# Kernel optimization log

Measured on AMD Instinct MI355X. Metric: run time of the kernel, lower is better.

Reference implementation:

```python
import jax, jax.numpy as jnp
import numpy as np

B, S, NT, D, NU = 1024, 200, 10000, 256, 100000
BETA_1 = 0.1


def setup_inputs() -> dict:
    key = jax.random.key(0)
    ks = jax.random.split(key, 6)
    user_id = jax.random.randint(ks[0], (B,), 0, NU)
    event_type = jax.random.randint(ks[1], (B, S), 0, NT + 1)  # 0 = pad
    adjacent_matrix = jax.random.uniform(ks[2], (NT, NT), dtype=jnp.float32)
    pop_encoding = jax.random.normal(ks[3], (NT + 1, D), dtype=jnp.float32)
    event_emb = jax.random.normal(ks[4], (NT + 1, D), dtype=jnp.float32) * 0.02
    user_emb = jax.random.normal(ks[5], (NU, D), dtype=jnp.float32) * 0.02
    return dict(user_id=user_id, event_type=event_type,
                adjacent_matrix=adjacent_matrix, pop_encoding=pop_encoding,
                evaluation=0, event_emb=event_emb, user_emb=user_emb)


def _l2norm(x, eps):
    # tf.nn.l2_normalize: x * rsqrt(max(sum(x^2), eps))
    return x * jax.lax.rsqrt(jnp.maximum(jnp.sum(x * x, axis=-1, keepdims=True), eps))


def reference(user_id, event_type, adjacent_matrix, pop_encoding, evaluation, event_emb, user_emb):
    non_pad = (event_type != 0).astype(jnp.float32)[..., None]          # [B,S,1]
    enc = event_emb[event_type]                                          # [B,S,D]
    usr = user_emb[user_id]                                              # [B,D]
    pop = pop_encoding[event_type] * non_pad                             # [B,S,D]
    # enc += sign(enc) * l2_normalize(user_output) (default eps 1e-12)
    enc = enc + jnp.sign(enc) * _l2norm(usr, 1e-12)[:, None, :]
    # per-sample adjacency: two-axis gather of the item-item matrix
    idx = jnp.where(event_type > 0, event_type - 1, 0)                   # [B,S]
    adj = adjacent_matrix[idx[:, :, None], idx[:, None, :]]              # [B,S,S]
    has_valid = (jnp.sum(event_type > 0, axis=1) > 0).astype(jnp.float32)
    adj = adj * has_valid[:, None, None]  # rows with all-pad stay zero, as in the loop
    output = jnp.mean(enc, axis=1)                                       # [B,D]
    user_embeddings = jnp.concatenate([output, jnp.mean(pop, axis=1) * BETA_1], axis=-1)  # [B,2D]
    if evaluation:
        item_encoding = event_emb[1:]                                    # [NT,D]
        scores = user_embeddings[:, :D] @ item_encoding.T
    else:
        item_encoding = jnp.concatenate([event_emb[1:], pop_encoding[1:] * BETA_1], axis=-1)  # [NT,2D]
        scores = user_embeddings @ item_encoding.T                       # [B,NT]
    prediction = jnp.tanh(_l2norm(scores, 1e-05))
    return prediction, user_embeddings, pop, adj
```

## Files before the change

### kernel.cpp

```cpp
#include <hip/hip_runtime.h>
#include <math.h>

#define NB 1024
#define NS 200
#define NTOK 10000
#define ND 256
#define BETA 0.1f

static constexpr size_t PRED_OFF = 0;
static constexpr size_t UE_OFF   = (size_t)NB * NTOK;
static constexpr size_t POP_OFF  = UE_OFF + (size_t)NB * 2 * ND;
static constexpr size_t ADJ_OFF  = POP_OFF + (size_t)NB * NS * ND;

static constexpr size_t WS_SIDX   = 0;
static constexpr size_t WS_HV     = WS_SIDX + (size_t)NB * NS;
static constexpr size_t WS_COUNTS = WS_HV + NB;
static constexpr size_t WS_OFFS   = WS_COUNTS + NTOK;
static constexpr size_t WS_CURSOR = WS_OFFS + NTOK + 1;
static constexpr size_t WS_PAIRS  = WS_CURSOR + NTOK;
static constexpr size_t WS_UEBF   = 440640;
static constexpr size_t WS_IEBF   = WS_UEBF + 262144;

typedef __attribute__((ext_vector_type(8))) short bf16x8;
typedef __attribute__((ext_vector_type(4))) float f32x4;

static __device__ inline unsigned short f2bf(float f) {
    unsigned int u = __float_as_uint(f);
    return (unsigned short)((u + 0x7fffu + ((u >> 16) & 1u)) >> 16);
}

__global__ __launch_bounds__(256) void k_embed(
    const int* __restrict__ user_id,
    const int* __restrict__ event_type,
    const float* __restrict__ pop_encoding,
    const float* __restrict__ event_emb,
    const float* __restrict__ user_emb,
    float* __restrict__ ue,
    unsigned short* __restrict__ ue_bf,
    float* __restrict__ pop)
{
    const int b  = blockIdx.x;
    const int t  = threadIdx.x;
    const int sg = t >> 6;
    const int tl = t & 63;

    const int uid = user_id[b];
    const float4 u4 = *(const float4*)&user_emb[(size_t)uid * ND + tl * 4];

    float ss = u4.x * u4.x + u4.y * u4.y + u4.z * u4.z + u4.w * u4.w;
    #pragma unroll
    for (int o = 32; o > 0; o >>= 1) ss += __shfl_xor(ss, o, 64);
    const float rn = rsqrtf(fmaxf(ss, 1e-12f));
    const float4 nu4 = {u4.x * rn, u4.y * rn, u4.z * rn, u4.w * rn};

    __shared__ int et_s[NS];
    if (t < NS) et_s[t] = event_type[(size_t)b * NS + t];
    __syncthreads();

    float4 eacc = {0.f, 0.f, 0.f, 0.f};
    float4 pacc = {0.f, 0.f, 0.f, 0.f};
    #pragma unroll 2
    for (int it = 0; it < NS / 4; ++it) {
        const int s  = sg + 4 * it;
        const int et = et_s[s];
        const float4 e = *(const float4*)&event_emb[(size_t)et * ND + tl * 4];
        float4 p = *(const float4*)&pop_encoding[(size_t)et * ND + tl * 4];
        const float z = (et != 0) ? 1.f : 0.f;
        p.x *= z; p.y *= z; p.z *= z; p.w *= z;
        eacc.x += e.x + ((e.x > 0.f) ? nu4.x : ((e.x < 0.f) ? -nu4.x : 0.f));
        eacc.y += e.y + ((e.y > 0.f) ? nu4.y : ((e.y < 0.f) ? -nu4.y : 0.f));
        eacc.z += e.z + ((e.z > 0.f) ? nu4.z : ((e.z < 0.f) ? -nu4.z : 0.f));
        eacc.w += e.w + ((e.w > 0.f) ? nu4.w : ((e.w < 0.f) ? -nu4.w : 0.f));
        pacc.x += p.x; pacc.y += p.y; pacc.z += p.z; pacc.w += p.w;
        const f32x4 pv = {p.x, p.y, p.z, p.w};
        __builtin_nontemporal_store(pv, (f32x4*)&pop[((size_t)b * NS + s) * ND + tl * 4]);
    }

    __shared__ __align__(16) float4 es[4][64];
    __shared__ __align__(16) float4 ps[4][64];
    es[sg][tl] = eacc;
    ps[sg][tl] = pacc;
    __syncthreads();

    if (t < 64) {
        float4 ef = es[0][t], pf = ps[0][t];
        #pragma unroll
        for (int w = 1; w < 4; ++w) {
            const float4 e2 = es[w][t], p2 = ps[w][t];
            ef.x += e2.x; ef.y += e2.y; ef.z += e2.z; ef.w += e2.w;
            pf.x += p2.x; pf.y += p2.y; pf.z += p2.z; pf.w += p2.w;
        }
        const float se = 1.f / NS, sp = BETA / NS;
        const float4 eo = {ef.x * se, ef.y * se, ef.z * se, ef.w * se};
        const float4 po = {pf.x * sp, pf.y * sp, pf.z * sp, pf.w * sp};
        *(float4*)&ue[(size_t)b * 512 + t * 4]       = eo;
        *(float4*)&ue[(size_t)b * 512 + 256 + t * 4] = po;
        ushort4 he = {f2bf(eo.x), f2bf(eo.y), f2bf(eo.z), f2bf(eo.w)};
        ushort4 hp = {f2bf(po.x), f2bf(po.y), f2bf(po.z), f2bf(po.w)};
        *(ushort4*)&ue_bf[(size_t)b * 512 + t * 4]       = he;
        *(ushort4*)&ue_bf[(size_t)b * 512 + 256 + t * 4] = hp;
    }
}

__global__ __launch_bounds__(256) void k_iebf(
    const float* __restrict__ ee,
    const float* __restrict__ pe,
    unsigned short* __restrict__ ie)
{
    const int idx = blockIdx.x * 256 + threadIdx.x;
    if (idx >= NTOK * 128) return;
    const int row = idx >> 7;
    const int kq  = idx & 127;
    float4 v; float sc;
    if (kq < 64) { v = *(const float4*)&ee[(size_t)(row + 1) * ND + kq * 4]; sc = 1.f; }
    else         { v = *(const float4*)&pe[(size_t)(row + 1) * ND + (kq - 64) * 4]; sc = BETA; }
    ushort4 h = {f2bf(v.x * sc), f2bf(v.y * sc), f2bf(v.z * sc), f2bf(v.w * sc)};
    *(ushort4*)&ie[(size_t)row * 512 + kq * 4] = h;
}

__global__ __launch_bounds__(256) void k_zero(int* __restrict__ counts)
{
    const int i = blockIdx.x * 256 + threadIdx.x;
    if (i < NTOK) counts[i] = 0;
}

__global__ __launch_bounds__(256) void k_prep(
    const int* __restrict__ event_type,
    int* __restrict__ sidx_all,
    float* __restrict__ hvf,
    int* __restrict__ counts)
{
    const int b = blockIdx.x;
    const int t = threadIdx.x;
    __shared__ int hv_s;
    if (t == 0) hv_s = 0;
    __syncthreads();
    if (t < NS) {
        const int et = event_type[(size_t)b * NS + t];
        const int r  = (et > 0) ? (et - 1) : 0;
        sidx_all[(size_t)b * NS + t] = r;
        if (et > 0) hv_s = 1;
        atomicAdd(&counts[r], 1);
    }
    __syncthreads();
    if (t == 0) hvf[b] = hv_s ? 1.f : 0.f;
}

#define SCAN_CHUNK 40
__global__ __launch_bounds__(256) void k_scan(
    const int* __restrict__ counts,
    int* __restrict__ offsets,
    int* __restrict__ cursor)
{
    const int t = threadIdx.x;
    int sum = 0;
    int local[SCAN_CHUNK];
    #pragma unroll
    for (int k = 0; k < SCAN_CHUNK; ++k) {
        const int idx = t * SCAN_CHUNK + k;
        const int c = (idx < NTOK) ? counts[idx] : 0;
        local[k] = c;
        sum += c;
    }
    __shared__ int part[256];
    part[t] = sum;
    __syncthreads();
    for (int o = 1; o < 256; o <<= 1) {
        const int v = (t >= o) ? part[t - o] : 0;
        __syncthreads();
        part[t] += v;
        __syncthreads();
    }
    int running = part[t] - sum;
    #pragma unroll
    for (int k = 0; k < SCAN_CHUNK; ++k) {
        const int idx = t * SCAN_CHUNK + k;
        if (idx < NTOK) {
            offsets[idx] = running;
            cursor[idx]  = running;
            running += local[k];
        }
    }
    if (t == 255) offsets[NTOK] = part[255];
}

__global__ __launch_bounds__(256) void k_scatter(
    const int* __restrict__ sidx_all,
    int* __restrict__ cursor,
    int* __restrict__ pairs)
{
    const int b = blockIdx.x;
    const int t = threadIdx.x;
    if (t < NS) {
        const int r = sidx_all[(size_t)b * NS + t];
        const int slot = atomicAdd(&cursor[r], 1);
        pairs[slot] = b * NS + t;
    }
}

__global__ __launch_bounds__(256) void k_adj2(
    const float* __restrict__ A,
    const int* __restrict__ sidx_all,
    const int* __restrict__ offsets,
    const int* __restrict__ pairs,
    const float* __restrict__ hvf,
    float* __restrict__ adj)
{
    const int r = blockIdx.x;
    const int t = threadIdx.x;
    const int p0 = offsets[r];
    const int n  = offsets[r + 1] - p0;
    if (n == 0) return;

    __shared__ __align__(16) float rowlds[NTOK];
    const float4* Arow = (const float4*)(A + (size_t)r * NTOK);
    #pragma unroll 4
    for (int l = t; l < NTOK / 4; l += 256)
        ((float4*)rowlds)[l] = Arow[l];
    __syncthreads();

    const int wave = t >> 6, lane = t & 63;
    for (int pi = wave; pi < n; pi += 4) {
        const int pv = pairs[p0 + pi];
        const int b  = pv / NS;
        const float hv = hvf[b];
        if (lane < 50) {
            const int4 c4 = *(const int4*)&sidx_all[(size_t)b * NS + lane * 4];
            f32x4 v;
            v.x = rowlds[c4.x] * hv;
            v.y = rowlds[c4.y] * hv;
            v.z = rowlds[c4.z] * hv;
            v.w = rowlds[c4.w] * hv;
            __builtin_nontemporal_store(v, (f32x4*)&adj[(size_t)pv * NS + lane * 4]);
        }
    }
}

#define GBM 128
#define GBN 128
#define GBK 32
#define LDK 40

__global__ __launch_bounds__(256) void k_gemm_mfma(
    const unsigned short* __restrict__ ue_bf,
    const unsigned short* __restrict__ ie_bf,
    float* __restrict__ scores)
{
    __shared__ __align__(16) unsigned short As[GBM * LDK];
    __shared__ __align__(16) unsigned short Bs[GBN * LDK];

    const int t  = threadIdx.x;
    const int bn = blockIdx.x, bm = blockIdx.y;
    const int m0 = bm * GBM, n0 = bn * GBN;

    const int wave = t >> 6, lane = t & 63;
    const int ww = wave & 1, wm = wave >> 1;
    const int lr = lane & 15;
    const int kg = lane >> 4;

    const int kq = t & 7;
    const int rq = t >> 3;

    f32x4 acc[4][4] = {};

    for (int k0 = 0; k0 < 512; k0 += GBK) {
        #pragma unroll
        for (int i = 0; i < 4; ++i) {
            const int r = rq + 32 * i;
            *(ushort4*)&As[r * LDK + kq * 4] =
                *(const ushort4*)&ue_bf[(size_t)(m0 + r) * 512 + k0 + kq * 4];
        }
        #pragma unroll
        for (int i = 0; i < 4; ++i) {
            const int r = rq + 32 * i;
            const int gn = n0 + r;
            ushort4 h = {0, 0, 0, 0};
            if (gn < NTOK)
                h = *(const ushort4*)&ie_bf[(size_t)gn * 512 + k0 + kq * 4];
            *(ushort4*)&Bs[r * LDK + kq * 4] = h;
        }
        __syncthreads();

        bf16x8 a[4], b[4];
        #pragma unroll
        for (int mf = 0; mf < 4; ++mf)
            a[mf] = *(const bf16x8*)&As[(wm * 64 + mf * 16 + lr) * LDK + kg * 8];
        #pragma unroll
        for (int nf = 0; nf < 4; ++nf)
            b[nf] = *(const bf16x8*)&Bs[(ww * 64 + nf * 16 + lr) * LDK + kg * 8];
        #pragma unroll
        for (int mf = 0; mf < 4; ++mf)
            #pragma unroll
            for (int nf = 0; nf < 4; ++nf)
                acc[mf][nf] = __builtin_amdgcn_mfma_f32_16x16x32_bf16(
                    a[mf], b[nf], acc[mf][nf], 0, 0, 0);
        __syncthreads();
    }

    #pragma unroll
    for (int mf = 0; mf < 4; ++mf) {
        const int row = m0 + wm * 64 + mf * 16 + kg * 4;
        #pragma unroll
        for (int nf = 0; nf < 4; ++nf) {
            const int col = n0 + ww * 64 + nf * 16 + lr;
            if (col < NTOK) {
                #pragma unroll
                for (int r = 0; r < 4; ++r)
                    scores[(size_t)(row + r) * NTOK + col] = acc[mf][nf][r];
            }
        }
    }
}

__global__ __launch_bounds__(256) void k_norm(float* __restrict__ scores)
{
    const int b = blockIdx.x;
    const int t = threadIdx.x;
    float4* row4 = (float4*)(scores + (size_t)b * NTOK);

    float ss = 0.f;
    for (int l = t; l < NTOK / 4; l += 256) {
        const float4 v = row4[l];
        ss += v.x * v.x + v.y * v.y + v.z * v.z + v.w * v.w;
    }
    #pragma unroll
    for (int o = 32; o > 0; o >>= 1) ss += __shfl_down(ss, o, 64);
    __shared__ float wss[4];
    const int wid = t >> 6, lane = t & 63;
    if (lane == 0) wss[wid] = ss;
    __syncthreads();
    const float tot = wss[0] + wss[1] + wss[2] + wss[3];
    const float rs = rsqrtf(fmaxf(tot, 1e-5f));

    for (int l = t; l < NTOK / 4; l += 256) {
        float4 v = row4[l];
        v.x = tanhf(v.x * rs); v.y = tanhf(v.y * rs);
        v.z = tanhf(v.z * rs); v.w = tanhf(v.w * rs);
        row4[l] = v;
    }
}

extern "C" void kernel_launch(void* const* d_in, const int* in_sizes, int n_in,
                              void* d_out, int out_size, void* d_ws, size_t ws_size,
                              hipStream_t stream) {
    const int*   user_id      = (const int*)d_in[0];
    const int*   event_type   = (const int*)d_in[1];
    const float* adjacent     = (const float*)d_in[2];
    const float* pop_encoding = (const float*)d_in[3];
    const float* event_emb    = (const float*)d_in[5];
    const float* user_emb     = (const float*)d_in[6];

    float* out  = (float*)d_out;
    float* pred = out + PRED_OFF;
    float* ue   = out + UE_OFF;
    float* pop  = out + POP_OFF;
    float* adj  = out + ADJ_OFF;

    int*   ws       = (int*)d_ws;
    int*   sidx_all = ws + WS_SIDX;
    float* hvf      = (float*)(ws + WS_HV);
    int*   counts   = ws + WS_COUNTS;
    int*   offsets  = ws + WS_OFFS;
    int*   cursor   = ws + WS_CURSOR;
    int*   pairs    = ws + WS_PAIRS;
    unsigned short* ue_bf = (unsigned short*)(ws + WS_UEBF);
    unsigned short* ie_bf = (unsigned short*)(ws + WS_IEBF);

    k_embed<<<NB, 256, 0, stream>>>(user_id, event_type, pop_encoding,
                                    event_emb, user_emb, ue, ue_bf, pop);
    k_iebf<<<(NTOK * 128 + 255) / 256, 256, 0, stream>>>(event_emb, pop_encoding, ie_bf);

    k_zero<<<(NTOK + 255) / 256, 256, 0, stream>>>(counts);
    k_prep<<<NB, 256, 0, stream>>>(event_type, sidx_all, hvf, counts);
    k_scan<<<1, 256, 0, stream>>>(counts, offsets, cursor);
    k_scatter<<<NB, 256, 0, stream>>>(sidx_all, cursor, pairs);
    k_adj2<<<NTOK, 256, 0, stream>>>(adjacent, sidx_all, offsets, pairs, hvf, adj);

    dim3 ggrid((NTOK + GBN - 1) / GBN, NB / GBM);
    k_gemm_mfma<<<ggrid, 256, 0, stream>>>(ue_bf, ie_bf, pred);
    k_norm<<<NB, 256, 0, stream>>>(pred);
}
```

Baseline: 319.8 us.

## Fuse prep kernels, widen adjacency blocks, and vectorize GEMM tile loads

The item bf16 conversion and the counts zeroing are merged into one launch, and the per-sample index/count/has-valid prep moves into the embedding kernel. This cuts two kernel launches and one extra pass over event_type. The adjacency kernel moves to 512 threads per block to load each row faster and handle more pairs at once. GEMM global-to-LDS loads are widened to 16-byte vectors. The hv_s flag is now read after a later barrier, so it stays correct, but 512-thread blocks with a 40KB LDS row may lower occupancy.

```diff
diff --git a/kernel.cpp b/kernel.cpp
--- a/kernel.cpp
+++ b/kernel.cpp
@@ -23,10 +23,34 @@
 
 typedef __attribute__((ext_vector_type(8))) short bf16x8;
 typedef __attribute__((ext_vector_type(4))) float f32x4;
+typedef __attribute__((ext_vector_type(8))) unsigned short u16x8;
 
 static __device__ inline unsigned short f2bf(float f) {
     unsigned int u = __float_as_uint(f);
     return (unsigned short)((u + 0x7fffu + ((u >> 16) & 1u)) >> 16);
+}
+
+__global__ __launch_bounds__(256) void k_pre(
+    const float* __restrict__ ee,
+    const float* __restrict__ pe,
+    unsigned short* __restrict__ ie,
+    int* __restrict__ counts)
+{
+    const int blk = blockIdx.x;
+    const int t = threadIdx.x;
+    if (blk < 5000) {
+        const int idx = blk * 256 + t;
+        const int row = idx >> 7;
+        const int kq  = idx & 127;
+        float4 v; float sc;
+        if (kq < 64) { v = *(const float4*)&ee[(size_t)(row + 1) * ND + kq * 4]; sc = 1.f; }
+        else         { v = *(const float4*)&pe[(size_t)(row + 1) * ND + (kq - 64) * 4]; sc = BETA; }
+        ushort4 h = {f2bf(v.x * sc), f2bf(v.y * sc), f2bf(v.z * sc), f2bf(v.w * sc)};
+        *(ushort4*)&ie[(size_t)row * 512 + kq * 4] = h;
+    } else {
+        const int i = (blk - 5000) * 256 + t;
+        if (i < NTOK) counts[i] = 0;
+    }
 }
 
 __global__ __launch_bounds__(256) void k_embed(
@@ -37,7 +61,10 @@
     const float* __restrict__ user_emb,
     float* __restrict__ ue,
     unsigned short* __restrict__ ue_bf,
-    float* __restrict__ pop)
+    float* __restrict__ pop,
+    int* __restrict__ sidx_all,
+    float* __restrict__ hvf,
+    int* __restrict__ counts)
 {
     const int b  = blockIdx.x;
     const int t  = threadIdx.x;
@@ -54,8 +81,18 @@
     const float4 nu4 = {u4.x * rn, u4.y * rn, u4.z * rn, u4.w * rn};
 
     __shared__ int et_s[NS];
+    __shared__ int hv_s;
+    if (t == 0) hv_s = 0;
     if (t < NS) et_s[t] = event_type[(size_t)b * NS + t];
     __syncthreads();
+
+    if (t < NS) {
+        const int et = et_s[t];
+        const int r  = (et > 0) ? (et - 1) : 0;
+        sidx_all[(size_t)b * NS + t] = r;
+        atomicAdd(&counts[r], 1);
+        if (et > 0) hv_s = 1;
+    }
 
     float4 eacc = {0.f, 0.f, 0.f, 0.f};
     float4 pacc = {0.f, 0.f, 0.f, 0.f};
@@ -82,67 +119,22 @@
     ps[sg][tl] = pacc;
     __syncthreads();
 
-    if (t < 64) {
-        float4 ef = es[0][t], pf = ps[0][t];
+    if (t < 128) {
+        const int half = t >> 6;
+        const int l2   = t & 63;
+        float4 f = half ? ps[0][l2] : es[0][l2];
         #pragma unroll
         for (int w = 1; w < 4; ++w) {
-            const float4 e2 = es[w][t], p2 = ps[w][t];
-            ef.x += e2.x; ef.y += e2.y; ef.z += e2.z; ef.w += e2.w;
-            pf.x += p2.x; pf.y += p2.y; pf.z += p2.z; pf.w += p2.w;
-        }
-        const float se = 1.f / NS, sp = BETA / NS;
-        const float4 eo = {ef.x * se, ef.y * se, ef.z * se, ef.w * se};
-        const float4 po = {pf.x * sp, pf.y * sp, pf.z * sp, pf.w * sp};
-        *(float4*)&ue[(size_t)b * 512 + t * 4]       = eo;
-        *(float4*)&ue[(size_t)b * 512 + 256 + t * 4] = po;
-        ushort4 he = {f2bf(eo.x), f2bf(eo.y), f2bf(eo.z), f2bf(eo.w)};
-        ushort4 hp = {f2bf(po.x), f2bf(po.y), f2bf(po.z), f2bf(po.w)};
-        *(ushort4*)&ue_bf[(size_t)b * 512 + t * 4]       = he;
-        *(ushort4*)&ue_bf[(size_t)b * 512 + 256 + t * 4] = hp;
-    }
-}
-
-__global__ __launch_bounds__(256) void k_iebf(
-    const float* __restrict__ ee,
-    const float* __restrict__ pe,
-    unsigned short* __restrict__ ie)
-{
-    const int idx = blockIdx.x * 256 + threadIdx.x;
-    if (idx >= NTOK * 128) return;
-    const int row = idx >> 7;
-    const int kq  = idx & 127;
-    float4 v; float sc;
-    if (kq < 64) { v = *(const float4*)&ee[(size_t)(row + 1) * ND + kq * 4]; sc = 1.f; }
-    else         { v = *(const float4*)&pe[(size_t)(row + 1) * ND + (kq - 64) * 4]; sc = BETA; }
-    ushort4 h = {f2bf(v.x * sc), f2bf(v.y * sc), f2bf(v.z * sc), f2bf(v.w * sc)};
-    *(ushort4*)&ie[(size_t)row * 512 + kq * 4] = h;
-}
-
-__global__ __launch_bounds__(256) void k_zero(int* __restrict__ counts)
-{
-    const int i = blockIdx.x * 256 + threadIdx.x;
-    if (i < NTOK) counts[i] = 0;
-}
-
-__global__ __launch_bounds__(256) void k_prep(
-    const int* __restrict__ event_type,
-    int* __restrict__ sidx_all,
-    float* __restrict__ hvf,
-    int* __restrict__ counts)
-{
-    const int b = blockIdx.x;
-    const int t = threadIdx.x;
-    __shared__ int hv_s;
-    if (t == 0) hv_s = 0;
-    __syncthreads();
-    if (t < NS) {
-        const int et = event_type[(size_t)b * NS + t];
-        const int r  = (et > 0) ? (et - 1) : 0;
-        sidx_all[(size_t)b * NS + t] = r;
-        if (et > 0) hv_s = 1;
-        atomicAdd(&counts[r], 1);
-    }
-    __syncthreads();
+            const float4 g = half ? ps[w][l2] : es[w][l2];
+            f.x += g.x; f.y += g.y; f.z += g.z; f.w += g.w;
+        }
+        const float sc = half ? (BETA / NS) : (1.f / NS);
+        const float4 o = {f.x * sc, f.y * sc, f.z * sc, f.w * sc};
+        const size_t off = (size_t)b * 512 + half * 256 + l2 * 4;
+        *(float4*)&ue[off] = o;
+        ushort4 h = {f2bf(o.x), f2bf(o.y), f2bf(o.z), f2bf(o.w)};
+        *(ushort4*)&ue_bf[off] = h;
+    }
     if (t == 0) hvf[b] = hv_s ? 1.f : 0.f;
 }
 
@@ -198,7 +190,7 @@
     }
 }
 
-__global__ __launch_bounds__(256) void k_adj2(
+__global__ __launch_bounds__(512) void k_adj2(
     const float* __restrict__ A,
     const int* __restrict__ sidx_all,
     const int* __restrict__ offsets,
@@ -214,13 +206,14 @@
 
     __shared__ __align__(16) float rowlds[NTOK];
     const float4* Arow = (const float4*)(A + (size_t)r * NTOK);
-    #pragma unroll 4
-    for (int l = t; l < NTOK / 4; l += 256)
+    #pragma unroll 5
+    for (int l = t; l < NTOK / 4; l += 512)
         ((float4*)rowlds)[l] = Arow[l];
     __syncthreads();
 
     const int wave = t >> 6, lane = t & 63;
-    for (int pi = wave; pi < n; pi += 4) {
+    #pragma unroll 2
+    for (int pi = wave; pi < n; pi += 8) {
         const int pv = pairs[p0 + pi];
         const int b  = pv / NS;
         const float hv = hvf[b];
@@ -258,26 +251,25 @@
     const int lr = lane & 15;
     const int kg = lane >> 4;
 
-    const int kq = t & 7;
-    const int rq = t >> 3;
-
     f32x4 acc[4][4] = {};
 
     for (int k0 = 0; k0 < 512; k0 += GBK) {
         #pragma unroll
-        for (int i = 0; i < 4; ++i) {
-            const int r = rq + 32 * i;
-            *(ushort4*)&As[r * LDK + kq * 4] =
-                *(const ushort4*)&ue_bf[(size_t)(m0 + r) * 512 + k0 + kq * 4];
-        }
-        #pragma unroll
-        for (int i = 0; i < 4; ++i) {
-            const int r = rq + 32 * i;
-            const int gn = n0 + r;
-            ushort4 h = {0, 0, 0, 0};
+        for (int i = 0; i < 2; ++i) {
+            const int c = t + 256 * i;
+            const int row = c >> 2, q = c & 3;
+            *(u16x8*)&As[row * LDK + q * 8] =
+                *(const u16x8*)&ue_bf[(size_t)(m0 + row) * 512 + k0 + q * 8];
+        }
+        #pragma unroll
+        for (int i = 0; i < 2; ++i) {
+            const int c = t + 256 * i;
+            const int row = c >> 2, q = c & 3;
+            const int gn = n0 + row;
+            u16x8 h = {0, 0, 0, 0, 0, 0, 0, 0};
             if (gn < NTOK)
-                h = *(const ushort4*)&ie_bf[(size_t)gn * 512 + k0 + kq * 4];
-            *(ushort4*)&Bs[r * LDK + kq * 4] = h;
+                h = *(const u16x8*)&ie_bf[(size_t)gn * 512 + k0 + q * 8];
+            *(u16x8*)&Bs[row * LDK + q * 8] = h;
         }
         __syncthreads();
 
@@ -366,15 +358,14 @@
     unsigned short* ue_bf = (unsigned short*)(ws + WS_UEBF);
     unsigned short* ie_bf = (unsigned short*)(ws + WS_IEBF);
 
+    k_pre<<<5000 + (NTOK + 255) / 256, 256, 0, stream>>>(event_emb, pop_encoding,
+                                                         ie_bf, counts);
     k_embed<<<NB, 256, 0, stream>>>(user_id, event_type, pop_encoding,
-                                    event_emb, user_emb, ue, ue_bf, pop);
-    k_iebf<<<(NTOK * 128 + 255) / 256, 256, 0, stream>>>(event_emb, pop_encoding, ie_bf);
-
-    k_zero<<<(NTOK + 255) / 256, 256, 0, stream>>>(counts);
-    k_prep<<<NB, 256, 0, stream>>>(event_type, sidx_all, hvf, counts);
+                                    event_emb, user_emb, ue, ue_bf, pop,
+                                    sidx_all, hvf, counts);
     k_scan<<<1, 256, 0, stream>>>(counts, offsets, cursor);
     k_scatter<<<NB, 256, 0, stream>>>(sidx_all, cursor, pairs);
-    k_adj2<<<NTOK, 256, 0, stream>>>(adjacent, sidx_all, offsets, pairs, hvf, adj);
+    k_adj2<<<NTOK, 512, 0, stream>>>(adjacent, sidx_all, offsets, pairs, hvf, adj);
 
     dim3 ggrid((NTOK + GBN - 1) / GBN, NB / GBM);
     k_gemm_mfma<<<ggrid, 256, 0, stream>>>(ue_bf, ie_bf, pred);
```

Result: no change. 316.2 us (-1.1%).
